# Kernel tuning notes

Hardware: AMD Instinct MI355X
Metric: run time of the kernel (lower is better)

Reference implementation:

```python
import jax, jax.numpy as jnp
import numpy as np

NB_HEAD = 4
SIZE_PER_HEAD = 50
D_MODEL = 200
B, S = 4, 4096


def setup_inputs() -> dict:
    key = jax.random.key(0)
    ks = jax.random.split(key, 7)
    q = jax.random.normal(ks[0], (B, S, D_MODEL), dtype=jnp.float32)
    k = jax.random.normal(ks[1], (B, S, D_MODEL), dtype=jnp.float32)
    v = jax.random.normal(ks[2], (B, S, D_MODEL), dtype=jnp.float32)
    # glorot-uniform-like init for weights
    def glorot(key, shape):
        lim = jnp.sqrt(6.0 / (shape[0] + shape[1])).astype(jnp.float32)
        return jax.random.uniform(key, shape, jnp.float32, -lim, lim)
    WQ = glorot(ks[3], (D_MODEL, SIZE_PER_HEAD))
    WK = glorot(ks[4], (D_MODEL, SIZE_PER_HEAD))
    WV = glorot(ks[5], (D_MODEL, SIZE_PER_HEAD))
    WO = glorot(ks[6], (NB_HEAD * SIZE_PER_HEAD, D_MODEL))
    return {"q": q, "k": k, "v": v, "WQ": WQ, "WK": WK, "WV": WV, "WO": WO}


def reference(q, k, v, WQ, WK, WV, WO):
    # The original per-head loop reuses the SAME WQ/WK/WV each iteration,
    # so every head output is identical. Compute attention once and tile.
    Qp = jnp.einsum('bsd,de->bse', q, WQ)  # [B,S,h]
    Kp = jnp.einsum('bsd,de->bse', k, WK)
    Vp = jnp.einsum('bsd,de->bse', v, WV)
    scale = 1.0 / jnp.sqrt(jnp.asarray(SIZE_PER_HEAD, dtype=Qp.dtype))
    A = jax.nn.softmax(jnp.einsum('bqe,bke->bqk', Qp, Kp) * scale, axis=-1)  # [B,S,S]
    O = jnp.einsum('bqk,bke->bqe', A, Vp)  # [B,S,h]
    O_concat = jnp.tile(O, (1, 1, NB_HEAD))  # [B,S,NB_HEAD*h]
    return jnp.einsum('bsf,fd->bsd', O_concat, WO)
```

## Files before the change

### kernel.cpp

```cpp
#include <hip/hip_runtime.h>
#include <hip/hip_bf16.h>


typedef short s4 __attribute__((ext_vector_type(4)));
typedef float f4 __attribute__((ext_vector_type(4)));

#define SLEN 4096
#define NB 4
#define DMODEL 200
#define HREAL 50
#define HP 64
#define DMP 208
#define KVB 64
#define QSCALE 0.20402789f

__device__ __forceinline__ short f2bf(float f) {
  unsigned u = __builtin_bit_cast(unsigned, f);
  u += 0x7FFFu + ((u >> 16) & 1u);
  return (short)(u >> 16);
}

__device__ __forceinline__ float fexp2(float x) { return __builtin_amdgcn_exp2f(x); }

__global__ void prep_weights(const float* __restrict__ WQ, const float* __restrict__ WK,
                             const float* __restrict__ WV, const float* __restrict__ WO,
                             short* __restrict__ wqt, short* __restrict__ wkt,
                             short* __restrict__ wvt, short* __restrict__ wot) {
  int id = blockIdx.x * 256 + threadIdx.x;
  const int NW = HP * DMP;
  if (id < 3 * NW) {
    int which = id / NW, rem = id % NW;
    int e = rem / DMP, d = rem % DMP;
    float v = 0.f;
    if (e < HREAL && d < DMODEL) {
      const float* W = (which == 0) ? WQ : (which == 1 ? WK : WV);
      v = W[d * HREAL + e];
      if (which == 0) v *= QSCALE;
    }
    short* T = (which == 0) ? wqt : (which == 1 ? wkt : wvt);
    T[e * DMP + d] = f2bf(v);
  } else if (id < 4 * NW) {
    int rem = id - 3 * NW;
    int dm = rem / HP, e = rem % HP;
    float v = 0.f;
    if (dm < DMODEL && e < HREAL) {
      v = WO[(e)*DMODEL + dm] + WO[(HREAL + e) * DMODEL + dm] +
          WO[(2 * HREAL + e) * DMODEL + dm] + WO[(3 * HREAL + e) * DMODEL + dm];
    }
    wot[dm * HP + e] = f2bf(v);
  }
}

__global__ __launch_bounds__(256) void proj_kernel(
    const float* __restrict__ q, const float* __restrict__ k, const float* __restrict__ v,
    const short* __restrict__ wqt, const short* __restrict__ wkt, const short* __restrict__ wvt,
    short* __restrict__ Qp, short* __restrict__ Kp, short* __restrict__ VpT) {
  const int mode = blockIdx.z;
  const float* X = (mode == 0) ? q : (mode == 1 ? k : v);
  const short* WT = (mode == 0) ? wqt : (mode == 1 ? wkt : wvt);
  const int lane = threadIdx.x & 63, wid = threadIdx.x >> 6;
  const int l15 = lane & 15, g = lane >> 4;
  const int sbase = blockIdx.x * 64 + wid * 16;
  const int row = sbase + l15;
  f4 acc[4] = {};
  for (int c = 0; c < 13; ++c) {
    int d0 = 16 * c + 4 * g;
    f4 a4 = {};
    if (d0 < DMODEL) a4 = *(const f4*)(X + (size_t)row * DMODEL + d0);
    s4 af;
#pragma unroll
    for (int j = 0; j < 4; ++j) af[j] = f2bf(a4[j]);
#pragma unroll
    for (int n = 0; n < 4; ++n) {
      s4 bf = *(const s4*)(WT + (16 * n + l15) * DMP + d0);
      acc[n] = __builtin_amdgcn_mfma_f32_16x16x16bf16_1k(af, bf, acc[n], 0, 0, 0);
    }
  }
  if (mode < 2) {
    short* OUT = (mode == 0) ? Qp : Kp;
#pragma unroll
    for (int n = 0; n < 4; ++n)
#pragma unroll
      for (int r = 0; r < 4; ++r) {
        int rr = sbase + 4 * g + r;
        OUT[rr * HP + 16 * n + l15] = f2bf(acc[n][r]);
      }
  } else {
#pragma unroll
    for (int n = 0; n < 4; ++n)
#pragma unroll
      for (int r = 0; r < 4; ++r) {
        int rr = sbase + 4 * g + r;
        int bb = rr >> 12, s = rr & 4095;
        VpT[((bb * HP) + 16 * n + l15) * SLEN + s] = f2bf(acc[n][r]);
      }
  }
}

__global__ __launch_bounds__(256, 6) void attn_kernel(
    const short* __restrict__ Qp, const short* __restrict__ Kp,
    const short* __restrict__ VpT, float* __restrict__ Mp,
    float* __restrict__ Lp, float* __restrict__ Op) {
  __shared__ __align__(16) char Klds[KVB * 128];
  __shared__ __align__(16) char Vlds[HP * 128];
  const int tid = threadIdx.x;
  const int lane = tid & 63, wid = tid >> 6;
  const int l15 = lane & 15, g = lane >> 4;
  const int b = blockIdx.y, z = blockIdx.z;
  const int nsplit = gridDim.z;
  const int qrow = blockIdx.x * 64 + wid * 16 + l15;
  const int ksw = (l15 & 7) << 4;

  s4 qf[4];
  {
    const short* qptr = Qp + (size_t)(b * SLEN + qrow) * HP + 4 * g;
#pragma unroll
    for (int c = 0; c < 4; ++c) qf[c] = *(const s4*)(qptr + 16 * c);
  }

  const int kr0 = l15 * 128 + ((8 * g) ^ ksw);
  const int kr1 = l15 * 128 + ((32 + 8 * g) ^ ksw);
  const int kr2 = l15 * 128 + ((64 + 8 * g) ^ ksw);
  const int kr3 = l15 * 128 + ((96 + 8 * g) ^ ksw);
  const int vb = l15 * 128 + ((8 * g) ^ ksw);

  const int cj0 = tid, cj1 = tid + 256;
  const int ci0 = (cj0 ^ ((cj0 >> 3) & 7)) * 16;
  const int ci1 = (cj1 ^ ((cj1 >> 3) & 7)) * 16;
  const int d0 = cj0 >> 3, d1 = cj1 >> 3;
  const int ch0 = ((cj0 & 7) ^ (d0 & 7)) * 16;
  const int ch1 = ((cj1 & 7) ^ (d1 & 7)) * 16;

  const int kv0 = z * (SLEN / nsplit);
  const char* kp0 = (const char*)Kp + (size_t)(b * SLEN + kv0) * 128 + ci0;
  const char* kp1 = (const char*)Kp + (size_t)(b * SLEN + kv0) * 128 + ci1;
  const char* vp0 =
      (const char*)VpT + ((size_t)(b * HP + d0) * SLEN + kv0) * 2 + ch0;
  const char* vp1 =
      (const char*)VpT + ((size_t)(b * HP + d1) * SLEN + kv0) * 2 + ch1;

  f4 rk0 = *(const f4*)kp0;
  f4 rk1 = *(const f4*)kp1;
  f4 rv0 = *(const f4*)vp0;
  f4 rv1 = *(const f4*)vp1;
  kp0 += KVB * 128;
  kp1 += KVB * 128;
  vp0 += KVB * 2;
  vp1 += KVB * 2;

  f4 o[4] = {};
  float m = -1e30f, lsum = 0.f;
  const int nsteps = SLEN / nsplit / KVB;
  for (int step = 0; step < nsteps; ++step) {
    __syncthreads();
    *(f4*)(Klds + tid * 16) = rk0;
    *(f4*)(Klds + tid * 16 + 4096) = rk1;
    *(f4*)(Vlds + tid * 16) = rv0;
    *(f4*)(Vlds + tid * 16 + 4096) = rv1;
    __syncthreads();
    if (step + 1 < nsteps) {
      rk0 = *(const f4*)kp0;
      rk1 = *(const f4*)kp1;
      rv0 = *(const f4*)vp0;
      rv1 = *(const f4*)vp1;
      kp0 += KVB * 128;
      kp1 += KVB * 128;
      vp0 += KVB * 2;
      vp1 += KVB * 2;
    }
#pragma unroll
    for (int tt = 0; tt < 4; ++tt) {
      f4 st = {};
      {
        s4 kf0 = *(const s4*)(Klds + kr0 + tt * 2048);
        s4 kf1 = *(const s4*)(Klds + kr1 + tt * 2048);
        s4 kf2 = *(const s4*)(Klds + kr2 + tt * 2048);
        s4 kf3 = *(const s4*)(Klds + kr3 + tt * 2048);
        st = __builtin_amdgcn_mfma_f32_16x16x16bf16_1k(kf0, qf[0], st, 0, 0, 0);
        st = __builtin_amdgcn_mfma_f32_16x16x16bf16_1k(kf1, qf[1], st, 0, 0, 0);
        st = __builtin_amdgcn_mfma_f32_16x16x16bf16_1k(kf2, qf[2], st, 0, 0, 0);
        st = __builtin_amdgcn_mfma_f32_16x16x16bf16_1k(kf3, qf[3], st, 0, 0, 0);
      }
      float tmax = fmaxf(fmaxf(st[0], st[1]), fmaxf(st[2], st[3]));
      if (__builtin_expect(__any(tmax > m + 8.0f), 0)) {
        float t = fmaxf(tmax, __shfl_xor(tmax, 16));
        t = fmaxf(t, __shfl_xor(t, 32));
        t = fmaxf(t, m);
        float corr = fexp2(m - t);
        lsum *= corr;
#pragma unroll
        for (int n = 0; n < 4; ++n) {
          o[n][0] *= corr;
          o[n][1] *= corr;
          o[n][2] *= corr;
          o[n][3] *= corr;
        }
        m = t;
      }
      float p0 = fexp2(st[0] - m), p1 = fexp2(st[1] - m);
      float p2 = fexp2(st[2] - m), p3 = fexp2(st[3] - m);
      lsum += (p0 + p1) + (p2 + p3);
      union {
        unsigned u[2];
        s4 s;
      } pu;
      asm("v_cvt_pk_bf16_f32 %0, %1, %2" : "=v"(pu.u[0]) : "v"(p0), "v"(p1));
      asm("v_cvt_pk_bf16_f32 %0, %1, %2" : "=v"(pu.u[1]) : "v"(p2), "v"(p3));
      s4 pf = pu.s;
      const char* vrow = Vlds + (vb ^ (tt << 5));
#pragma unroll
      for (int n = 0; n < 4; ++n) {
        s4 vf = *(const s4*)(vrow + n * 2048);
        o[n] = __builtin_amdgcn_mfma_f32_16x16x16bf16_1k(vf, pf, o[n], 0, 0, 0);
      }
    }
  }
  lsum += __shfl_xor(lsum, 16);
  lsum += __shfl_xor(lsum, 32);
  const int rowg = b * SLEN + qrow;
  const int NR = NB * SLEN;
  if (lane < 16) {
    Mp[z * NR + rowg] = m;
    Lp[z * NR + rowg] = lsum;
  }
  float* op = Op + ((size_t)z * NR + rowg) * HP;
#pragma unroll
  for (int n = 0; n < 4; ++n) *(f4*)(op + 16 * n + 4 * g) = o[n];
}

template <int NSPLIT>
__global__ __launch_bounds__(256) void combineproj_kernel(
    const float* __restrict__ Mp, const float* __restrict__ Lp,
    const float* __restrict__ Op, const short* __restrict__ wot,
    float* __restrict__ out) {
  const int lane = threadIdx.x & 63, wid = threadIdx.x >> 6;
  const int l15 = lane & 15, g = lane >> 4;
  const int sbase = blockIdx.x * 64 + wid * 16;
  const int row = sbase + l15;
  const int NR = NB * SLEN;
  float mm = -1e30f;
#pragma unroll
  for (int s = 0; s < NSPLIT; ++s) mm = fmaxf(mm, Mp[s * NR + row]);
  float w[NSPLIT];
  float L = 0.f;
#pragma unroll
  for (int s = 0; s < NSPLIT; ++s) {
    w[s] = fexp2(Mp[s * NR + row] - mm);
    L += w[s] * Lp[s * NR + row];
  }
  float inv = 1.0f / L;
  s4 af[4];
#pragma unroll
  for (int c = 0; c < 4; ++c) {
    f4 acc = {};
#pragma unroll
    for (int s = 0; s < NSPLIT; ++s) {
      f4 vv = *(const f4*)(Op + ((size_t)s * NR + row) * HP + 16 * c + 4 * g);
      acc[0] += w[s] * vv[0];
      acc[1] += w[s] * vv[1];
      acc[2] += w[s] * vv[2];
      acc[3] += w[s] * vv[3];
    }
#pragma unroll
    for (int r = 0; r < 4; ++r) af[c][r] = f2bf(acc[r] * inv);
  }
  for (int n = 0; n < 13; ++n) {
    f4 acc = {};
    const short* brow = wot + (16 * n + l15) * HP + 4 * g;
#pragma unroll
    for (int c = 0; c < 4; ++c) {
      s4 bf = *(const s4*)(brow + 16 * c);
      acc = __builtin_amdgcn_mfma_f32_16x16x16bf16_1k(af[c], bf, acc, 0, 0, 0);
    }
    int dm = 16 * n + l15;
    if (dm < DMODEL) {
#pragma unroll
      for (int r = 0; r < 4; ++r) {
        int rr = sbase + 4 * g + r;
        out[(size_t)rr * DMODEL + dm] = acc[r];
      }
    }
  }
}

extern "C" void kernel_launch(void* const* d_in, const int* in_sizes, int n_in,
                              void* d_out, int out_size, void* d_ws, size_t ws_size,
                              hipStream_t stream) {
  const float* q = (const float*)d_in[0];
  const float* k = (const float*)d_in[1];
  const float* v = (const float*)d_in[2];
  const float* WQ = (const float*)d_in[3];
  const float* WK = (const float*)d_in[4];
  const float* WV = (const float*)d_in[5];
  const float* WO = (const float*)d_in[6];
  float* out = (float*)d_out;
  char* ws = (char*)d_ws;

  const size_t MB2 = 2097152;
  const size_t NR = (size_t)NB * SLEN;
  size_t need8 = 131072 + 4 * MB2 + 8 * NR * 4 * 2 + 8 * NR * HP * 4;
  int nsplit = (ws_size >= need8) ? 8 : 4;

  short* wqt = (short*)(ws + 0);
  short* wkt = (short*)(ws + 32768);
  short* wvt = (short*)(ws + 65536);
  short* wot = (short*)(ws + 98304);
  short* Qp = (short*)(ws + 131072);
  short* Kp = (short*)(ws + 131072 + MB2);
  short* VpT = (short*)(ws + 131072 + 2 * MB2);
  float* Mp = (float*)(ws + 131072 + 4 * MB2);
  float* Lp = Mp + nsplit * NR;
  float* Op = Lp + nsplit * NR;

  prep_weights<<<dim3(208), dim3(256), 0, stream>>>(WQ, WK, WV, WO, wqt, wkt, wvt, wot);
  proj_kernel<<<dim3(256, 1, 3), dim3(256), 0, stream>>>(q, k, v, wqt, wkt, wvt, Qp, Kp, VpT);
  attn_kernel<<<dim3(64, NB, nsplit), dim3(256), 0, stream>>>(Qp, Kp, VpT, Mp, Lp, Op);
  if (nsplit == 8)
    combineproj_kernel<8><<<dim3(256), dim3(256), 0, stream>>>(Mp, Lp, Op, wot, out);
  else
    combineproj_kernel<4><<<dim3(256), dim3(256), 0, stream>>>(Mp, Lp, Op, wot, out);
}
```

Baseline: 76.38 us.

## Process two 16-row query tiles per wave to reuse K/V LDS fragments

Each wave now handles 32 query rows as two independent 16-row tiles, A and B, each with its own online-softmax state. Every K and V fragment read from LDS feeds two MFMAs, so per-wave LDS traffic and the KV staging done per block are halved relative to compute. The grid's x dimension is halved to match, and the launch bound drops from 6 to 4 blocks per SIMD to make room for the extra registers. s_setprio is raised around the MFMA groups to favour matrix issue. In exchange there are fewer blocks and lower occupancy, which leaves less room to hide latency.

```diff
diff --git a/kernel.cpp b/kernel.cpp
--- a/kernel.cpp
+++ b/kernel.cpp
@@ -97,7 +97,7 @@
   }
 }
 
-__global__ __launch_bounds__(256, 6) void attn_kernel(
+__global__ __launch_bounds__(256, 4) void attn_kernel(
     const short* __restrict__ Qp, const short* __restrict__ Kp,
     const short* __restrict__ VpT, float* __restrict__ Mp,
     float* __restrict__ Lp, float* __restrict__ Op) {
@@ -108,14 +108,19 @@
   const int l15 = lane & 15, g = lane >> 4;
   const int b = blockIdx.y, z = blockIdx.z;
   const int nsplit = gridDim.z;
-  const int qrow = blockIdx.x * 64 + wid * 16 + l15;
+  const int qrowA = blockIdx.x * 128 + wid * 32 + l15;
+  const int qrowB = qrowA + 16;
   const int ksw = (l15 & 7) << 4;
 
-  s4 qf[4];
+  s4 qfA[4], qfB[4];
   {
-    const short* qptr = Qp + (size_t)(b * SLEN + qrow) * HP + 4 * g;
-#pragma unroll
-    for (int c = 0; c < 4; ++c) qf[c] = *(const s4*)(qptr + 16 * c);
+    const short* qpa = Qp + (size_t)(b * SLEN + qrowA) * HP + 4 * g;
+    const short* qpb = Qp + (size_t)(b * SLEN + qrowB) * HP + 4 * g;
+#pragma unroll
+    for (int c = 0; c < 4; ++c) {
+      qfA[c] = *(const s4*)(qpa + 16 * c);
+      qfB[c] = *(const s4*)(qpb + 16 * c);
+    }
   }
 
   const int kr0 = l15 * 128 + ((8 * g) ^ ksw);
@@ -148,8 +153,9 @@
   vp0 += KVB * 2;
   vp1 += KVB * 2;
 
-  f4 o[4] = {};
-  float m = -1e30f, lsum = 0.f;
+  f4 oA[4] = {}, oB[4] = {};
+  float mA = -1e30f, lsumA = 0.f;
+  float mB = -1e30f, lsumB = 0.f;
   const int nsteps = SLEN / nsplit / KVB;
   for (int step = 0; step < nsteps; ++step) {
     __syncthreads();
@@ -170,62 +176,94 @@
     }
 #pragma unroll
     for (int tt = 0; tt < 4; ++tt) {
-      f4 st = {};
+      f4 stA = {}, stB = {};
       {
         s4 kf0 = *(const s4*)(Klds + kr0 + tt * 2048);
         s4 kf1 = *(const s4*)(Klds + kr1 + tt * 2048);
         s4 kf2 = *(const s4*)(Klds + kr2 + tt * 2048);
         s4 kf3 = *(const s4*)(Klds + kr3 + tt * 2048);
-        st = __builtin_amdgcn_mfma_f32_16x16x16bf16_1k(kf0, qf[0], st, 0, 0, 0);
-        st = __builtin_amdgcn_mfma_f32_16x16x16bf16_1k(kf1, qf[1], st, 0, 0, 0);
-        st = __builtin_amdgcn_mfma_f32_16x16x16bf16_1k(kf2, qf[2], st, 0, 0, 0);
-        st = __builtin_amdgcn_mfma_f32_16x16x16bf16_1k(kf3, qf[3], st, 0, 0, 0);
-      }
-      float tmax = fmaxf(fmaxf(st[0], st[1]), fmaxf(st[2], st[3]));
-      if (__builtin_expect(__any(tmax > m + 8.0f), 0)) {
-        float t = fmaxf(tmax, __shfl_xor(tmax, 16));
+        __builtin_amdgcn_s_setprio(1);
+        stA = __builtin_amdgcn_mfma_f32_16x16x16bf16_1k(kf0, qfA[0], stA, 0, 0, 0);
+        stB = __builtin_amdgcn_mfma_f32_16x16x16bf16_1k(kf0, qfB[0], stB, 0, 0, 0);
+        stA = __builtin_amdgcn_mfma_f32_16x16x16bf16_1k(kf1, qfA[1], stA, 0, 0, 0);
+        stB = __builtin_amdgcn_mfma_f32_16x16x16bf16_1k(kf1, qfB[1], stB, 0, 0, 0);
+        stA = __builtin_amdgcn_mfma_f32_16x16x16bf16_1k(kf2, qfA[2], stA, 0, 0, 0);
+        stB = __builtin_amdgcn_mfma_f32_16x16x16bf16_1k(kf2, qfB[2], stB, 0, 0, 0);
+        stA = __builtin_amdgcn_mfma_f32_16x16x16bf16_1k(kf3, qfA[3], stA, 0, 0, 0);
+        stB = __builtin_amdgcn_mfma_f32_16x16x16bf16_1k(kf3, qfB[3], stB, 0, 0, 0);
+        __builtin_amdgcn_s_setprio(0);
+      }
+      float tmaxA = fmaxf(fmaxf(stA[0], stA[1]), fmaxf(stA[2], stA[3]));
+      if (__builtin_expect(__any(tmaxA > mA + 8.0f), 0)) {
+        float t = fmaxf(tmaxA, __shfl_xor(tmaxA, 16));
         t = fmaxf(t, __shfl_xor(t, 32));
-        t = fmaxf(t, m);
-        float corr = fexp2(m - t);
-        lsum *= corr;
+        t = fmaxf(t, mA);
+        float corr = fexp2(mA - t);
+        lsumA *= corr;
 #pragma unroll
         for (int n = 0; n < 4; ++n) {
-          o[n][0] *= corr;
-          o[n][1] *= corr;
-          o[n][2] *= corr;
-          o[n][3] *= corr;
+          oA[n][0] *= corr; oA[n][1] *= corr; oA[n][2] *= corr; oA[n][3] *= corr;
         }
-        m = t;
-      }
-      float p0 = fexp2(st[0] - m), p1 = fexp2(st[1] - m);
-      float p2 = fexp2(st[2] - m), p3 = fexp2(st[3] - m);
-      lsum += (p0 + p1) + (p2 + p3);
-      union {
-        unsigned u[2];
-        s4 s;
-      } pu;
-      asm("v_cvt_pk_bf16_f32 %0, %1, %2" : "=v"(pu.u[0]) : "v"(p0), "v"(p1));
-      asm("v_cvt_pk_bf16_f32 %0, %1, %2" : "=v"(pu.u[1]) : "v"(p2), "v"(p3));
-      s4 pf = pu.s;
+        mA = t;
+      }
+      float pa0 = fexp2(stA[0] - mA), pa1 = fexp2(stA[1] - mA);
+      float pa2 = fexp2(stA[2] - mA), pa3 = fexp2(stA[3] - mA);
+      lsumA += (pa0 + pa1) + (pa2 + pa3);
+      union { unsigned u[2]; s4 s; } puA;
+      asm("v_cvt_pk_bf16_f32 %0, %1, %2" : "=v"(puA.u[0]) : "v"(pa0), "v"(pa1));
+      asm("v_cvt_pk_bf16_f32 %0, %1, %2" : "=v"(puA.u[1]) : "v"(pa2), "v"(pa3));
+      s4 pfA = puA.s;
+      float tmaxB = fmaxf(fmaxf(stB[0], stB[1]), fmaxf(stB[2], stB[3]));
+      if (__builtin_expect(__any(tmaxB > mB + 8.0f), 0)) {
+        float t = fmaxf(tmaxB, __shfl_xor(tmaxB, 16));
+        t = fmaxf(t, __shfl_xor(t, 32));
+        t = fmaxf(t, mB);
+        float corr = fexp2(mB - t);
+        lsumB *= corr;
+#pragma unroll
+        for (int n = 0; n < 4; ++n) {
+          oB[n][0] *= corr; oB[n][1] *= corr; oB[n][2] *= corr; oB[n][3] *= corr;
+        }
+        mB = t;
+      }
+      float pb0 = fexp2(stB[0] - mB), pb1 = fexp2(stB[1] - mB);
+      float pb2 = fexp2(stB[2] - mB), pb3 = fexp2(stB[3] - mB);
+      lsumB += (pb0 + pb1) + (pb2 + pb3);
+      union { unsigned u[2]; s4 s; } puB;
+      asm("v_cvt_pk_bf16_f32 %0, %1, %2" : "=v"(puB.u[0]) : "v"(pb0), "v"(pb1));
+      asm("v_cvt_pk_bf16_f32 %0, %1, %2" : "=v"(puB.u[1]) : "v"(pb2), "v"(pb3));
+      s4 pfB = puB.s;
       const char* vrow = Vlds + (vb ^ (tt << 5));
+      __builtin_amdgcn_s_setprio(1);
 #pragma unroll
       for (int n = 0; n < 4; ++n) {
         s4 vf = *(const s4*)(vrow + n * 2048);
-        o[n] = __builtin_amdgcn_mfma_f32_16x16x16bf16_1k(vf, pf, o[n], 0, 0, 0);
-      }
-    }
-  }
-  lsum += __shfl_xor(lsum, 16);
-  lsum += __shfl_xor(lsum, 32);
-  const int rowg = b * SLEN + qrow;
+        oA[n] = __builtin_amdgcn_mfma_f32_16x16x16bf16_1k(vf, pfA, oA[n], 0, 0, 0);
+        oB[n] = __builtin_amdgcn_mfma_f32_16x16x16bf16_1k(vf, pfB, oB[n], 0, 0, 0);
+      }
+      __builtin_amdgcn_s_setprio(0);
+    }
+  }
+  lsumA += __shfl_xor(lsumA, 16);
+  lsumA += __shfl_xor(lsumA, 32);
+  lsumB += __shfl_xor(lsumB, 16);
+  lsumB += __shfl_xor(lsumB, 32);
+  const int rowgA = b * SLEN + qrowA;
+  const int rowgB = b * SLEN + qrowB;
   const int NR = NB * SLEN;
   if (lane < 16) {
-    Mp[z * NR + rowg] = m;
-    Lp[z * NR + rowg] = lsum;
-  }
-  float* op = Op + ((size_t)z * NR + rowg) * HP;
-#pragma unroll
-  for (int n = 0; n < 4; ++n) *(f4*)(op + 16 * n + 4 * g) = o[n];
+    Mp[z * NR + rowgA] = mA;
+    Lp[z * NR + rowgA] = lsumA;
+    Mp[z * NR + rowgB] = mB;
+    Lp[z * NR + rowgB] = lsumB;
+  }
+  float* opA = Op + ((size_t)z * NR + rowgA) * HP;
+  float* opB = Op + ((size_t)z * NR + rowgB) * HP;
+#pragma unroll
+  for (int n = 0; n < 4; ++n) {
+    *(f4*)(opA + 16 * n + 4 * g) = oA[n];
+    *(f4*)(opB + 16 * n + 4 * g) = oB[n];
+  }
 }
 
 template <int NSPLIT>
@@ -314,7 +352,7 @@
 
   prep_weights<<<dim3(208), dim3(256), 0, stream>>>(WQ, WK, WV, WO, wqt, wkt, wvt, wot);
   proj_kernel<<<dim3(256, 1, 3), dim3(256), 0, stream>>>(q, k, v, wqt, wkt, wvt, Qp, Kp, VpT);
-  attn_kernel<<<dim3(64, NB, nsplit), dim3(256), 0, stream>>>(Qp, Kp, VpT, Mp, Lp, Op);
+  attn_kernel<<<dim3(32, NB, nsplit), dim3(256), 0, stream>>>(Qp, Kp, VpT, Mp, Lp, Op);
   if (nsplit == 8)
     combineproj_kernel<8><<<dim3(256), dim3(256), 0, stream>>>(Mp, Lp, Op, wot, out);
   else
```

New measurement: 73.21 us. 4.2% less time.
